# Optimization experiments

Measured on AMD Instinct MI355X. Metric: run time of the kernel, lower is better.

## Reference

```python
import jax, jax.numpy as jnp
import numpy as np

B, SQ, SK, D = 16, 2048, 2048, 64


def setup_inputs() -> dict:
    key = jax.random.key(0)
    k1, k2, k3, k4 = jax.random.split(key, 4)
    return {
        "query": jax.random.normal(k1, (B, SQ, D), dtype=jnp.float32),
        "key": jax.random.normal(k2, (B, SK, D), dtype=jnp.float32),
        "value": jax.random.normal(k3, (B, SK, D), dtype=jnp.float32),
        "mask": jax.random.randint(k4, (B, SQ, SK), 0, 2).astype(bool),
    }


def reference(query, key, value, mask):
    # score = Q K^T / sqrt(D); masked positions -> -inf
    scale = 1.0 / jnp.sqrt(jnp.asarray(query.shape[-1], query.dtype))
    score = jnp.einsum("bqd,bkd->bqk", query, key) * scale  # [B, SQ, SK]
    score = jnp.where(mask, -jnp.inf, score)
    attn = jax.nn.softmax(score, axis=-1)
    context = jnp.einsum("bqk,bkd->bqd", attn, value)  # [B, SQ, D]
    return (context, attn)
```

## Files before the change

kernel.cpp:

```cpp
#include <hip/hip_runtime.h>
#include <hip/hip_bf16.h>

typedef __attribute__((ext_vector_type(8)))  __bf16 bf16x8;
typedef __attribute__((ext_vector_type(4)))  __bf16 bf16x4;
typedef __attribute__((ext_vector_type(16))) float  f32x16;

namespace {
constexpr int kB  = 16;
constexpr int kSQ = 2048;
constexpr int kSK = 2048;
constexpr int kD  = 64;
constexpr int kQB = 32;
constexpr int kNW = 8;
constexpr int kKPW = kSK / kNW;
constexpr int kLdsP = kQB * kSK * 2;
constexpr int kLdsTot = kLdsP + kNW * kQB * 4;
constexpr float kScaleLog2e = 0.18033688011112042f;
}

__global__ __launch_bounds__(512, 2)
void sdpa_fused(const float* __restrict__ Qg, const float* __restrict__ Kg,
                const float* __restrict__ Vg, const int* __restrict__ Mg,
                float* __restrict__ ctxOut, float* __restrict__ attnOut)
{
  __shared__ __align__(16) char lds[kLdsTot];
  float* sums  = reinterpret_cast<float*>(lds + kLdsP);
  float* cpart = reinterpret_cast<float*>(lds);

  const int tid  = threadIdx.x;
  const int wid  = tid >> 6;
  const int lane = tid & 63;
  const int l31  = lane & 31;
  const int lh   = lane >> 5;

  const int wg = (blockIdx.x & 7) * 128 + (blockIdx.x >> 3);
  const int b  = wg >> 6;
  const int q0 = (wg & 63) * kQB;

  const float* Qb = Qg + (size_t)b * kSQ * kD;
  const float* Kb = Kg + (size_t)b * kSK * kD;
  const float* Vb = Vg + (size_t)b * kSK * kD;
  const int*   Mb = Mg + (size_t)b * kSQ * kSK;

  bf16x8 qf[4];
  {
    const float* qp = Qb + (q0 + l31) * kD + lh * 8;
#pragma unroll
    for (int s = 0; s < 4; ++s) {
#pragma unroll
      for (int e = 0; e < 8; ++e) qf[s][e] = (__bf16)qp[s * 16 + e];
    }
  }

  float lsum[16];
#pragma unroll
  for (int r = 0; r < 16; ++r) lsum[r] = 0.f;

  const int kbase = wid * kKPW;
  for (int kt = 0; kt < kKPW / 32; ++kt) {
    const int k0 = kbase + kt * 32;
    f32x16 acc;
#pragma unroll
    for (int r = 0; r < 16; ++r) acc[r] = 0.f;
    const float* kp = Kb + (k0 + l31) * kD + lh * 8;
#pragma unroll
    for (int s = 0; s < 4; ++s) {
      bf16x8 kf;
#pragma unroll
      for (int e = 0; e < 8; ++e) kf[e] = (__bf16)kp[s * 16 + e];
      acc = __builtin_amdgcn_mfma_f32_32x32x16_bf16(qf[s], kf, acc, 0, 0, 0);
    }
    const int col = k0 + l31;
    const int* mp = Mb + (size_t)q0 * kSK + col;
#pragma unroll
    for (int r = 0; r < 16; ++r) {
      const int row = (r & 3) + 8 * (r >> 2) + 4 * lh;
      const int mv  = mp[row * kSK];
      const float pv = mv ? 0.f : exp2f(acc[r] * kScaleLog2e);
      lsum[r] += pv;
      const int byte = ((row << 12) + (col << 1)) ^ ((row & 7) << 4);
      *reinterpret_cast<__bf16*>(lds + byte) = (__bf16)pv;
    }
  }

#pragma unroll
  for (int m = 1; m < 32; m <<= 1) {
#pragma unroll
    for (int r = 0; r < 16; ++r) lsum[r] += __shfl_xor(lsum[r], m, 64);
  }
  if (l31 == 0) {
#pragma unroll
    for (int r = 0; r < 16; ++r) {
      const int row = (r & 3) + 8 * (r >> 2) + 4 * lh;
      sums[wid * kQB + row] = lsum[r];
    }
  }
  __syncthreads();

#pragma unroll
  for (int rr = 0; rr < 4; ++rr) {
    const int row = wid * 4 + rr;
    float l = 0.f;
#pragma unroll
    for (int w = 0; w < kNW; ++w) l += sums[w * kQB + row];
    const float inv = 1.0f / l;
    const int xorm = (row & 7) << 4;
    float* arow = attnOut + ((size_t)b * kSQ + q0 + row) * kSK;
    for (int c0 = lane * 4; c0 < kSK; c0 += 256) {
      const int byte = ((row << 12) + (c0 << 1)) ^ xorm;
      const bf16x4 p4 = *reinterpret_cast<const bf16x4*>(lds + byte);
      float4 o;
      o.x = (float)p4[0] * inv;
      o.y = (float)p4[1] * inv;
      o.z = (float)p4[2] * inv;
      o.w = (float)p4[3] * inv;
      *reinterpret_cast<float4*>(arow + c0) = o;
    }
  }

  const int d0  = (wid >> 2) * 32;
  const int kb2 = (wid & 3) * 512;
  f32x16 cacc;
#pragma unroll
  for (int r = 0; r < 16; ++r) cacc[r] = 0.f;
  for (int ks = 0; ks < 512 / 16; ++ks) {
    const int k0 = kb2 + ks * 16;
    const int abyte = ((l31 << 12) + ((k0 + lh * 8) << 1)) ^ ((l31 & 7) << 4);
    const bf16x8 af = *reinterpret_cast<const bf16x8*>(lds + abyte);
    bf16x8 vf;
    const float* vp = Vb + (size_t)(k0 + lh * 8) * kD + d0 + l31;
#pragma unroll
    for (int e = 0; e < 8; ++e) vf[e] = (__bf16)vp[e * kD];
    cacc = __builtin_amdgcn_mfma_f32_32x32x16_bf16(af, vf, cacc, 0, 0, 0);
  }
  __syncthreads();

#pragma unroll
  for (int r = 0; r < 16; ++r) {
    const int row = (r & 3) + 8 * (r >> 2) + 4 * lh;
    cpart[wid * (kQB * 32) + row * 32 + l31] = cacc[r];
  }
  __syncthreads();

  {
    const int m = tid >> 4;
    const int c = (tid & 15) * 4;
    const int team = (c >= 32) ? 4 : 0;
    const int cc = c & 31;
    float4 o = make_float4(0.f, 0.f, 0.f, 0.f);
#pragma unroll
    for (int w = 0; w < 4; ++w) {
      const float4 pv = *reinterpret_cast<const float4*>(
          cpart + (team + w) * (kQB * 32) + m * 32 + cc);
      o.x += pv.x; o.y += pv.y; o.z += pv.z; o.w += pv.w;
    }
    float l = 0.f;
#pragma unroll
    for (int w = 0; w < kNW; ++w) l += sums[w * kQB + m];
    const float inv = 1.0f / l;
    o.x *= inv; o.y *= inv; o.z *= inv; o.w *= inv;
    *reinterpret_cast<float4*>(ctxOut + ((size_t)b * kSQ + q0 + m) * kD + c) = o;
  }
}

extern "C" void kernel_launch(void* const* d_in, const int* in_sizes, int n_in,
                              void* d_out, int out_size, void* d_ws, size_t ws_size,
                              hipStream_t stream)
{
  const float* Q = (const float*)d_in[0];
  const float* K = (const float*)d_in[1];
  const float* V = (const float*)d_in[2];
  const int*   M = (const int*)d_in[3];
  float* ctx  = (float*)d_out;
  float* attn = (float*)d_out + (size_t)kB * kSQ * kD;

  dim3 grid(kB * (kSQ / kQB));
  dim3 block(512);
  hipLaunchKernelGGL(sdpa_fused, grid, block, 0, stream, Q, K, V, M, ctx, attn);
}
```

Measured before the change: 168.9 us.

## Halve query tile to 16 rows with 16x16x32 MFMA and higher occupancy

Shrinks the per-block query tile from 32 to 16 rows, which halves the LDS buffer holding the bf16 probability tile, and raises launch bounds to allow four blocks per CU. Both GEMM phases switch from 32x32x16 to 16x16x32 MFMA tiles. The PV stage is repartitioned so each wave covers its own key range across all 64 output columns instead of a d-half by key-quarter split, and reduces the eight partials through LDS. Each block also switches to the raw exp2 builtin. The aim is more resident waves to hide latency on mask loads and attention stores, at the cost of reloading K and V for twice as many blocks and using smaller MFMA tiles.

```diff
diff --git a/kernel.cpp b/kernel.cpp
--- a/kernel.cpp
+++ b/kernel.cpp
@@ -1,24 +1,23 @@
 #include <hip/hip_runtime.h>
 #include <hip/hip_bf16.h>
 
-typedef __attribute__((ext_vector_type(8)))  __bf16 bf16x8;
-typedef __attribute__((ext_vector_type(4)))  __bf16 bf16x4;
-typedef __attribute__((ext_vector_type(16))) float  f32x16;
+typedef __attribute__((ext_vector_type(8))) __bf16 bf16x8;
+typedef __attribute__((ext_vector_type(4))) __bf16 bf16x4;
+typedef __attribute__((ext_vector_type(4))) float  f32x4;
 
 namespace {
 constexpr int kB  = 16;
 constexpr int kSQ = 2048;
 constexpr int kSK = 2048;
 constexpr int kD  = 64;
-constexpr int kQB = 32;
+constexpr int kQB = 16;
 constexpr int kNW = 8;
-constexpr int kKPW = kSK / kNW;
 constexpr int kLdsP = kQB * kSK * 2;
 constexpr int kLdsTot = kLdsP + kNW * kQB * 4;
 constexpr float kScaleLog2e = 0.18033688011112042f;
 }
 
-__global__ __launch_bounds__(512, 2)
+__global__ __launch_bounds__(512, 4)
 void sdpa_fused(const float* __restrict__ Qg, const float* __restrict__ Kg,
                 const float* __restrict__ Vg, const int* __restrict__ Mg,
                 float* __restrict__ ctxOut, float* __restrict__ attnOut)
@@ -30,53 +29,47 @@
   const int tid  = threadIdx.x;
   const int wid  = tid >> 6;
   const int lane = tid & 63;
-  const int l31  = lane & 31;
-  const int lh   = lane >> 5;
+  const int l15  = lane & 15;
+  const int kg   = lane >> 4;
 
-  const int wg = (blockIdx.x & 7) * 128 + (blockIdx.x >> 3);
-  const int b  = wg >> 6;
-  const int q0 = (wg & 63) * kQB;
+  const int wg = (blockIdx.x & 7) * 256 + (blockIdx.x >> 3);
+  const int b  = wg >> 7;
+  const int q0 = (wg & 127) * kQB;
 
   const float* Qb = Qg + (size_t)b * kSQ * kD;
   const float* Kb = Kg + (size_t)b * kSK * kD;
   const float* Vb = Vg + (size_t)b * kSK * kD;
   const int*   Mb = Mg + (size_t)b * kSQ * kSK;
 
-  bf16x8 qf[4];
+  bf16x8 qf[2];
   {
-    const float* qp = Qb + (q0 + l31) * kD + lh * 8;
+    const float* qp = Qb + (q0 + l15) * kD + kg * 8;
 #pragma unroll
-    for (int s = 0; s < 4; ++s) {
+    for (int s = 0; s < 2; ++s)
 #pragma unroll
-      for (int e = 0; e < 8; ++e) qf[s][e] = (__bf16)qp[s * 16 + e];
-    }
+      for (int e = 0; e < 8; ++e) qf[s][e] = (__bf16)qp[s * 32 + e];
   }
 
-  float lsum[16];
+  float lsum[4] = {0.f, 0.f, 0.f, 0.f};
+  for (int kt = 0; kt < 16; ++kt) {
+    const int k0 = wid * 256 + kt * 16;
+    f32x4 acc = {0.f, 0.f, 0.f, 0.f};
+    const float* kp = Kb + (size_t)(k0 + l15) * kD + kg * 8;
 #pragma unroll
-  for (int r = 0; r < 16; ++r) lsum[r] = 0.f;
-
-  const int kbase = wid * kKPW;
-  for (int kt = 0; kt < kKPW / 32; ++kt) {
-    const int k0 = kbase + kt * 32;
-    f32x16 acc;
-#pragma unroll
-    for (int r = 0; r < 16; ++r) acc[r] = 0.f;
-    const float* kp = Kb + (k0 + l31) * kD + lh * 8;
-#pragma unroll
-    for (int s = 0; s < 4; ++s) {
+    for (int s = 0; s < 2; ++s) {
       bf16x8 kf;
 #pragma unroll
-      for (int e = 0; e < 8; ++e) kf[e] = (__bf16)kp[s * 16 + e];
-      acc = __builtin_amdgcn_mfma_f32_32x32x16_bf16(qf[s], kf, acc, 0, 0, 0);
+      for (int e = 0; e < 8; ++e) kf[e] = (__bf16)kp[s * 32 + e];
+      acc = __builtin_amdgcn_mfma_f32_16x16x32_bf16(qf[s], kf, acc, 0, 0, 0);
     }
-    const int col = k0 + l31;
-    const int* mp = Mb + (size_t)q0 * kSK + col;
+    const int col = k0 + l15;
+    const int* mp = Mb + (size_t)(q0 + kg * 4) * kSK + col;
 #pragma unroll
-    for (int r = 0; r < 16; ++r) {
-      const int row = (r & 3) + 8 * (r >> 2) + 4 * lh;
-      const int mv  = mp[row * kSK];
-      const float pv = mv ? 0.f : exp2f(acc[r] * kScaleLog2e);
+    for (int r = 0; r < 4; ++r) {
+      const int row = kg * 4 + r;
+      const int mv  = mp[(size_t)r * kSK];
+      const float pv =
+          mv ? 0.f : __builtin_amdgcn_exp2f(acc[r] * kScaleLog2e);
       lsum[r] += pv;
       const int byte = ((row << 12) + (col << 1)) ^ ((row & 7) << 4);
       *reinterpret_cast<__bf16*>(lds + byte) = (__bf16)pv;
@@ -84,22 +77,18 @@
   }
 
 #pragma unroll
-  for (int m = 1; m < 32; m <<= 1) {
+  for (int m = 1; m < 16; m <<= 1)
 #pragma unroll
-    for (int r = 0; r < 16; ++r) lsum[r] += __shfl_xor(lsum[r], m, 64);
-  }
-  if (l31 == 0) {
+    for (int r = 0; r < 4; ++r) lsum[r] += __shfl_xor(lsum[r], m, 64);
+  if (l15 == 0) {
 #pragma unroll
-    for (int r = 0; r < 16; ++r) {
-      const int row = (r & 3) + 8 * (r >> 2) + 4 * lh;
-      sums[wid * kQB + row] = lsum[r];
-    }
+    for (int r = 0; r < 4; ++r) sums[wid * kQB + kg * 4 + r] = lsum[r];
   }
   __syncthreads();
 
 #pragma unroll
-  for (int rr = 0; rr < 4; ++rr) {
-    const int row = wid * 4 + rr;
+  for (int rr = 0; rr < 2; ++rr) {
+    const int row = wid * 2 + rr;
     float l = 0.f;
 #pragma unroll
     for (int w = 0; w < kNW; ++w) l += sums[w * kQB + row];
@@ -118,48 +107,47 @@
     }
   }
 
-  const int d0  = (wid >> 2) * 32;
-  const int kb2 = (wid & 3) * 512;
-  f32x16 cacc;
+  f32x4 cacc[4];
 #pragma unroll
-  for (int r = 0; r < 16; ++r) cacc[r] = 0.f;
-  for (int ks = 0; ks < 512 / 16; ++ks) {
-    const int k0 = kb2 + ks * 16;
-    const int abyte = ((l31 << 12) + ((k0 + lh * 8) << 1)) ^ ((l31 & 7) << 4);
+  for (int nt = 0; nt < 4; ++nt) cacc[nt] = f32x4{0.f, 0.f, 0.f, 0.f};
+  for (int ks = 0; ks < 8; ++ks) {
+    const int kk = wid * 256 + ks * 32;
+    const int abyte = ((l15 << 12) + ((kk + kg * 8) << 1)) ^ ((l15 & 7) << 4);
     const bf16x8 af = *reinterpret_cast<const bf16x8*>(lds + abyte);
-    bf16x8 vf;
-    const float* vp = Vb + (size_t)(k0 + lh * 8) * kD + d0 + l31;
 #pragma unroll
-    for (int e = 0; e < 8; ++e) vf[e] = (__bf16)vp[e * kD];
-    cacc = __builtin_amdgcn_mfma_f32_32x32x16_bf16(af, vf, cacc, 0, 0, 0);
+    for (int nt = 0; nt < 4; ++nt) {
+      bf16x8 vf;
+      const float* vp = Vb + (size_t)(kk + kg * 8) * kD + nt * 16 + l15;
+#pragma unroll
+      for (int e = 0; e < 8; ++e) vf[e] = (__bf16)vp[e * kD];
+      cacc[nt] = __builtin_amdgcn_mfma_f32_16x16x32_bf16(af, vf, cacc[nt], 0, 0, 0);
+    }
   }
   __syncthreads();
 
 #pragma unroll
-  for (int r = 0; r < 16; ++r) {
-    const int row = (r & 3) + 8 * (r >> 2) + 4 * lh;
-    cpart[wid * (kQB * 32) + row * 32 + l31] = cacc[r];
-  }
+  for (int nt = 0; nt < 4; ++nt)
+#pragma unroll
+    for (int r = 0; r < 4; ++r)
+      cpart[wid * (kQB * kD) + (kg * 4 + r) * kD + nt * 16 + l15] = cacc[nt][r];
   __syncthreads();
 
-  {
-    const int m = tid >> 4;
-    const int c = (tid & 15) * 4;
-    const int team = (c >= 32) ? 4 : 0;
-    const int cc = c & 31;
+  if (tid < kQB * 16) {
+    const int row = tid >> 4;
+    const int c   = (tid & 15) * 4;
     float4 o = make_float4(0.f, 0.f, 0.f, 0.f);
 #pragma unroll
-    for (int w = 0; w < 4; ++w) {
+    for (int w = 0; w < kNW; ++w) {
       const float4 pv = *reinterpret_cast<const float4*>(
-          cpart + (team + w) * (kQB * 32) + m * 32 + cc);
+          cpart + w * (kQB * kD) + row * kD + c);
       o.x += pv.x; o.y += pv.y; o.z += pv.z; o.w += pv.w;
     }
     float l = 0.f;
 #pragma unroll
-    for (int w = 0; w < kNW; ++w) l += sums[w * kQB + m];
+    for (int w = 0; w < kNW; ++w) l += sums[w * kQB + row];
     const float inv = 1.0f / l;
     o.x *= inv; o.y *= inv; o.z *= inv; o.w *= inv;
-    *reinterpret_cast<float4*>(ctxOut + ((size_t)b * kSQ + q0 + m) * kD + c) = o;
+    *reinterpret_cast<float4*>(ctxOut + ((size_t)b * kSQ + q0 + row) * kD + c) = o;
   }
 }
 
```

Measured after the change: 237.1 us. 1.4x slower.
